# Kernel tuning notes

Measured on AMD Instinct MI355X. Metric: run time of the kernel, lower is better.

The kernel has to match this reference:

```python
import math
import jax, jax.numpy as jnp
import numpy as np

EPS = 1e-7
TOPK = 10
FACTOR_IOU = 6.0
FACTOR_CLS = 0.5


def ciou(b1, b2):
    """Complete IoU. b1, b2 broadcastable [..., 4] boxes (x1,y1,x2,y2)."""
    xi1 = jnp.maximum(b1[..., 0], b2[..., 0])
    yi1 = jnp.maximum(b1[..., 1], b2[..., 1])
    xi2 = jnp.minimum(b1[..., 2], b2[..., 2])
    yi2 = jnp.minimum(b1[..., 3], b2[..., 3])
    inter = jnp.clip(xi2 - xi1, 0) * jnp.clip(yi2 - yi1, 0)
    a1 = (b1[..., 2] - b1[..., 0]) * (b1[..., 3] - b1[..., 1])
    a2 = (b2[..., 2] - b2[..., 0]) * (b2[..., 3] - b2[..., 1])
    union = a1 + a2 - inter
    iou = inter / (union + EPS)
    cx1 = (b1[..., 2] + b1[..., 0]) * 0.5
    cy1 = (b1[..., 3] + b1[..., 1]) * 0.5
    cx2 = (b2[..., 2] + b2[..., 0]) * 0.5
    cy2 = (b2[..., 3] + b2[..., 1]) * 0.5
    cent = (cx1 - cx2) ** 2 + (cy1 - cy2) ** 2
    cw = jnp.maximum(b1[..., 2], b2[..., 2]) - jnp.minimum(b1[..., 0], b2[..., 0])
    ch = jnp.maximum(b1[..., 3], b2[..., 3]) - jnp.minimum(b1[..., 1], b2[..., 1])
    diag = cw ** 2 + ch ** 2 + EPS
    diou = iou - cent / diag
    arctan = (jnp.arctan((b1[..., 2] - b1[..., 0]) / (b1[..., 3] - b1[..., 1] + EPS))
              - jnp.arctan((b2[..., 2] - b2[..., 0]) / (b2[..., 3] - b2[..., 1] + EPS)))
    v = (4.0 / math.pi ** 2) * arctan ** 2
    alpha = jax.lax.stop_gradient(v / (v - iou + 1.0 + EPS))
    return diou - alpha * v


def box_matcher(target, predict_cls, predict_bbox, anchors, class_num):
    """target [B,T,5]; predict_cls [B,A,C] logits; predict_bbox [B,A,4]; anchors [A,2].
    Returns anchor_matched_targets [B,A,C+4], valid_mask [B,A] bool."""
    B, T = target.shape[0], target.shape[1]
    A = anchors.shape[0]
    tcls = jnp.clip(target[..., 0].astype(jnp.int32), 0)        # [B,T]
    tbox = target[..., 1:5]                                       # [B,T,4]

    # grid mask: anchor center inside target box
    ax = anchors[None, None, :, 0]
    ay = anchors[None, None, :, 1]
    grid_mask = ((tbox[:, :, None, 0] < ax) & (ax < tbox[:, :, None, 2])
                 & (tbox[:, :, None, 1] < ay) & (ay < tbox[:, :, None, 3]))  # [B,T,A]

    # pairwise CIoU target x anchor
    iou_mat = jnp.clip(ciou(tbox[:, :, None, :], predict_bbox[:, None, :, :]), 0.0, 1.0)  # [B,T,A]

    # class prob of each target's class at each anchor
    pc = jax.nn.sigmoid(predict_cls)                              # [B,A,C]
    idx_bta = jnp.broadcast_to(tcls[:, :, None], (B, T, A))
    cls_mat = jnp.take_along_axis(pc.transpose(0, 2, 1), idx_bta, axis=1)  # [B,T,A]

    target_matrix = grid_mask * iou_mat ** FACTOR_IOU * cls_mat ** FACTOR_CLS

    # top-k targets per anchor (topk over anchor axis, as in source)
    vals, idx = jax.lax.top_k(target_matrix, TOPK)                # [B,T,K]
    bi = jnp.arange(B)[:, None, None]
    ti = jnp.arange(T)[None, :, None]
    topk_targets = jnp.zeros_like(target_matrix).at[bi, ti, idx].set(vals)
    topk_mask = (topk_targets > 0).astype(jnp.int32)              # [B,T,A]

    # resolve anchors assigned to multiple targets by max IoU
    duplicates = (topk_mask.sum(1, keepdims=True) > 1)            # [B,1,A]
    max_idx = jax.nn.one_hot(jnp.argmax(iou_mat, axis=1), T, dtype=jnp.int32).transpose(0, 2, 1)  # [B,T,A]
    topk_mask = jnp.where(duplicates, max_idx, topk_mask)
    unique_indices = jnp.argmax(topk_mask, axis=1)                # [B,A]
    valid = topk_mask.sum(1)                                      # [B,A]

    align_bbox = jnp.take_along_axis(tbox, jnp.broadcast_to(unique_indices[:, :, None], (B, A, 4)), axis=1)  # [B,A,4]
    align_cls_idx = jnp.take_along_axis(tcls, unique_indices, axis=1)  # [B,A]
    align_cls = jax.nn.one_hot(align_cls_idx, class_num, dtype=target_matrix.dtype)  # [B,A,C]

    iou_m = iou_mat * topk_mask
    tm_m = target_matrix * topk_mask
    max_target = tm_m.max(axis=-1, keepdims=True)                 # [B,T,1]
    max_iou = iou_m.max(axis=-1, keepdims=True)                   # [B,T,1]
    normalize_term = tm_m / (max_target + 1e-9) * max_iou         # [B,T,A]
    normalize_term = jnp.take_along_axis(normalize_term.transpose(0, 2, 1),
                                         unique_indices[:, :, None], axis=2)  # [B,A,1]
    align_cls = align_cls * normalize_term * valid[:, :, None].astype(align_cls.dtype)
    anchor_matched_targets = jnp.concatenate([align_cls, align_bbox], axis=-1)
    return anchor_matched_targets, (valid > 0)


def setup_inputs() -> dict:
    key = jax.random.key(0)
    ks = jax.random.split(key, 6)
    B, T, C = 32, 64, 80
    img = 640.0
    cells = []
    for s in (8, 16, 32):
        n = 640 // s
        xs = (np.arange(n, dtype=np.float32) + 0.5) * s
        gx, gy = np.meshgrid(xs, xs)
        cells.append(np.stack([gx.ravel(), gy.ravel()], axis=1))
    anchors = jnp.asarray(np.concatenate(cells, 0), dtype=jnp.float32)  # [8400,2]
    A = anchors.shape[0]
    cls = jax.random.randint(ks[0], (B, T, 1), 0, C).astype(jnp.float32)
    cxy = jax.random.uniform(ks[1], (B, T, 2)) * img
    wh = jax.random.uniform(ks[2], (B, T, 2)) * 160.0 + 8.0
    tbox = jnp.concatenate([cxy - wh / 2, cxy + wh / 2], axis=-1)
    target = jnp.concatenate([cls, tbox], axis=-1)                # [B,T,5]
    predict_cls = jax.random.normal(ks[3], (B, A, C), dtype=jnp.float32)
    pcxy = anchors[None] + (jax.random.uniform(ks[4], (B, A, 2)) - 0.5) * 32.0
    pwh = jax.random.uniform(ks[5], (B, A, 2)) * 128.0 + 8.0
    predict_bbox = jnp.concatenate([pcxy - pwh / 2, pcxy + pwh / 2], axis=-1)  # [B,A,4]
    return {"target": target, "predict_cls": predict_cls,
            "predict_bbox": predict_bbox, "anchors": anchors}


def reference(target, predict_cls, predict_bbox, anchors):
    C = predict_cls.shape[-1]
    # matcher runs on detached predictions (as in the torch source)
    amt, valid = box_matcher(target,
                             jax.lax.stop_gradient(predict_cls),
                             jax.lax.stop_gradient(predict_bbox),
                             anchors, C)
    targets_cls = amt[..., :C]                                    # [B,A,C]
    targets_bbox = amt[..., C:]                                   # [B,A,4]
    cls_norm = jnp.maximum(targets_cls.sum(), 1.0)
    box_norm = targets_cls.sum(-1)                                # [B,A]

    # BCE-with-logits, sum / cls_norm
    x, t = predict_cls, targets_cls
    bce = jnp.maximum(x, 0) - x * t + jnp.log1p(jnp.exp(-jnp.abs(x)))
    loss_cls = bce.sum() / cls_norm

    # CIoU box loss over valid anchors (elementwise == diag of picked pairwise)
    iou_e = ciou(predict_bbox, targets_bbox)                      # [B,A]
    loss_iou = ((1.0 - iou_e) * box_norm * valid).sum() / cls_norm

    return jnp.stack([loss_iou, loss_cls])
```

## Files before the change

### kernel.cpp

```cpp
#include <hip/hip_runtime.h>
#include <climits>
#include <cmath>


#define NB 32
#define NT 64
#define NA 8400
#define NC 80
#define KTOP 10
#define NE (NT * KTOP)
#define CAP 1024
#define EPSF 1e-7f
#define INV_PI2 0.40528473456935108577f
#define LOG2E_F 1.44269504088896340736f
#define LN2_F   0.69314718055994530942f

__device__ __forceinline__ float atan_wh(float x1, float y1, float x2, float y2) {
  return atanf((x2 - x1) / (y2 - y1 + EPSF));
}

__device__ __forceinline__ float ciou_pair(
    float ax1, float ay1, float ax2, float ay2, float atA,
    float bx1, float by1, float bx2, float by2, float atB)
{
  float xi1 = fmaxf(ax1, bx1), yi1 = fmaxf(ay1, by1);
  float xi2 = fminf(ax2, bx2), yi2 = fminf(ay2, by2);
  float inter = fmaxf(xi2 - xi1, 0.f) * fmaxf(yi2 - yi1, 0.f);
  float a1 = (ax2 - ax1) * (ay2 - ay1);
  float a2 = (bx2 - bx1) * (by2 - by1);
  float iou = inter / (a1 + a2 - inter + EPSF);
  float dcx = (ax2 + ax1) * 0.5f - (bx2 + bx1) * 0.5f;
  float dcy = (ay2 + ay1) * 0.5f - (by2 + by1) * 0.5f;
  float cent = dcx * dcx + dcy * dcy;
  float cw = fmaxf(ax2, bx2) - fminf(ax1, bx1);
  float ch = fmaxf(ay2, by2) - fminf(ay1, by1);
  float diag = cw * cw + ch * ch + EPSF;
  float dv = atA - atB;
  float v = INV_PI2 * dv * dv;
  float alpha = v / (v - iou + 1.f + EPSF);
  return iou - cent / diag - alpha * v;
}

__device__ __forceinline__ float softplus_fast(float x) {
  float e = exp2f(-LOG2E_F * fabsf(x));
  float l = __log2f(1.f + e);
  return fmaxf(x, 0.f) + LN2_F * l;
}

__global__ __launch_bounds__(256) void k_topk(
    const float* __restrict__ target,
    const float* __restrict__ pcls,
    const float* __restrict__ pbox,
    float* __restrict__ top_val, int* __restrict__ top_idx,
    float* __restrict__ top_iou,
    unsigned* __restrict__ mtg, unsigned* __restrict__ mig)
{
  int row = blockIdx.x;
  int tid = threadIdx.x;
  if (tid == 0) { mtg[row] = 0u; mig[row] = 0u; }
  int b = row >> 6;
  const float* tg = target + (size_t)row * 5;
  float tcf = tg[0];
  float x1 = tg[1], y1 = tg[2], x2 = tg[3], y2 = tg[4];
  int tc = (int)tcf; tc = tc < 0 ? 0 : (tc > NC - 1 ? NC - 1 : tc);
  float atan_t = atan_wh(x1, y1, x2, y2);

  __shared__ int s_n;
  __shared__ float s_val[CAP];
  __shared__ int s_idx[CAP];
  __shared__ float xw_v[4];  __shared__ int xw_a[4];
  __shared__ float w_val[KTOP]; __shared__ int w_idx[KTOP];
  if (tid == 0) s_n = 0;
  __syncthreads();

  const float* pb_b = pbox + (size_t)b * NA * 4;
  const float* pc_b = pcls + (size_t)b * NA * NC;

#define LEVEL_LOOP(S, N, BASE)                                              \
  {                                                                         \
    const float s = (float)(S);                                             \
    \
    int ix0 = (int)floorf(x1 / s - 0.5f); ix0 = ix0 < 0 ? 0 : ix0;          \
    int ix1 = (int)ceilf (x2 / s - 0.5f); ix1 = ix1 > (N)-1 ? (N)-1 : ix1;  \
    int iy0 = (int)floorf(y1 / s - 0.5f); iy0 = iy0 < 0 ? 0 : iy0;          \
    int iy1 = (int)ceilf (y2 / s - 0.5f); iy1 = iy1 > (N)-1 ? (N)-1 : iy1;  \
    int w = ix1 - ix0 + 1; w = w < 0 ? 0 : w;                               \
    int h = iy1 - iy0 + 1; h = h < 0 ? 0 : h;                               \
    int cnt = w * h;                                                        \
    for (int k = tid; k < cnt; k += 256) {                                  \
      int ix = ix0 + k % w;                                                 \
      int iy = iy0 + k / w;                                                 \
      float anx = (ix + 0.5f) * s;                                          \
      float any_ = (iy + 0.5f) * s;                                         \
      if (x1 < anx && anx < x2 && y1 < any_ && any_ < y2) {                 \
        int a = (BASE) + iy * (N) + ix;                                     \
        float4 bb = ((const float4*)pb_b)[a];                               \
        float c = ciou_pair(x1, y1, x2, y2, atan_t, bb.x, bb.y, bb.z, bb.w, \
                            atan_wh(bb.x, bb.y, bb.z, bb.w));               \
        float io = fminf(fmaxf(c, 0.f), 1.f);                               \
        float i2 = io * io;                                                 \
        float i6 = i2 * i2 * i2;                                            \
        float sc = pc_b[(size_t)a * NC + tc];                               \
        float sig = 1.f / (1.f + expf(-sc));                                \
        float tm = i6 * sqrtf(sig);                                         \
        int slot = atomicAdd(&s_n, 1);                                      \
        if (slot < CAP) { s_val[slot] = tm; s_idx[slot] = a; }              \
      }                                                                     \
    }                                                                       \
  }
  LEVEL_LOOP(8, 80, 0)
  LEVEL_LOOP(16, 40, 6400)
  LEVEL_LOOP(32, 20, 8000)
#undef LEVEL_LOOP
  __syncthreads();
  int n = s_n; if (n > CAP) n = CAP;

  float v0 = -1.f, v1 = -1.f, v2 = -1.f, v3 = -1.f;
  int a0 = INT_MAX, a1 = INT_MAX, a2 = INT_MAX, a3 = INT_MAX;
  if (tid < n)       { v0 = s_val[tid];       a0 = s_idx[tid]; }
  if (tid + 256 < n) { v1 = s_val[tid + 256]; a1 = s_idx[tid + 256]; }
  if (tid + 512 < n) { v2 = s_val[tid + 512]; a2 = s_idx[tid + 512]; }
  if (tid + 768 < n) { v3 = s_val[tid + 768]; a3 = s_idx[tid + 768]; }

  for (int k = 0; k < KTOP; k++) {
    float bv = v0; int ba = a0;
    if (v1 > bv || (v1 == bv && a1 < ba)) { bv = v1; ba = a1; }
    if (v2 > bv || (v2 == bv && a2 < ba)) { bv = v2; ba = a2; }
    if (v3 > bv || (v3 == bv && a3 < ba)) { bv = v3; ba = a3; }
#pragma unroll
    for (int off = 32; off > 0; off >>= 1) {
      float ov = __shfl_xor(bv, off); int oa = __shfl_xor(ba, off);
      if (ov > bv || (ov == bv && oa < ba)) { bv = ov; ba = oa; }
    }
    if ((tid & 63) == 0) { xw_v[tid >> 6] = bv; xw_a[tid >> 6] = ba; }
    __syncthreads();
    float fv = xw_v[0]; int fa = xw_a[0];
    { float ov = xw_v[1]; int oa = xw_a[1];
      if (ov > fv || (ov == fv && oa < fa)) { fv = ov; fa = oa; } }
    { float ov = xw_v[2]; int oa = xw_a[2];
      if (ov > fv || (ov == fv && oa < fa)) { fv = ov; fa = oa; } }
    { float ov = xw_v[3]; int oa = xw_a[3];
      if (ov > fv || (ov == fv && oa < fa)) { fv = ov; fa = oa; } }
    if (tid == 0) { w_val[k] = fv; w_idx[k] = fa; }
    if (a0 == fa) { v0 = -1.f; a0 = INT_MAX; }
    if (a1 == fa) { v1 = -1.f; a1 = INT_MAX; }
    if (a2 == fa) { v2 = -1.f; a2 = INT_MAX; }
    if (a3 == fa) { v3 = -1.f; a3 = INT_MAX; }
    __syncthreads();
  }

  if (tid < KTOP) {
    int k = tid;
    int ai = w_idx[k]; float v = w_val[k];
    float io = 0.f;
    if (ai != INT_MAX && v > 0.f) {
      float4 bb = ((const float4*)pb_b)[ai];
      float c = ciou_pair(x1, y1, x2, y2, atan_t, bb.x, bb.y, bb.z, bb.w,
                          atan_wh(bb.x, bb.y, bb.z, bb.w));
      io = fminf(fmaxf(c, 0.f), 1.f);
    } else { ai = -1; v = 0.f; }
    size_t o = (size_t)row * KTOP + k;
    top_val[o] = v; top_idx[o] = ai; top_iou[o] = io;
  }
}

__global__ __launch_bounds__(256) void k_resolve(
    const float* __restrict__ target, const float* __restrict__ pcls,
    const float* __restrict__ pbox, const float* __restrict__ anchors,
    const float* __restrict__ top_val, const int* __restrict__ top_idx,
    const float* __restrict__ top_iou,
    float* __restrict__ as_tm, float* __restrict__ as_x,
    float* __restrict__ as_cio, int* __restrict__ as_u,
    unsigned* __restrict__ mtg, unsigned* __restrict__ mig)
{
  int gid = blockIdx.x * 256 + threadIdx.x;
  int entry = gid >> 6;
  int lane = threadIdx.x & 63;
  int b = entry / NE;
  int el = entry - b * NE;

  const float* bv = top_val + (size_t)b * NE;
  const int* bix = top_idx + (size_t)b * NE;
  float v = bv[el];
  int a = bix[el];

  bool dead = (v <= 0.f);
  int cnt = 0, first = NE;
  if (!dead) {
    for (int s = lane; s < NE; s += 64) {
      float v2 = bv[s]; int a2 = bix[s];
      if (v2 > 0.f && a2 == a) { cnt++; if (s < first) first = s; }
    }
    for (int off = 32; off > 0; off >>= 1) {
      cnt += __shfl_xor(cnt, off);
      int of = __shfl_xor(first, off);
      first = of < first ? of : first;
    }
    if (first != el) dead = true;
  }
  if (dead) {
    if (lane == 0) { as_tm[entry] = 0.f; as_x[entry] = 0.f;
                     as_cio[entry] = 0.f; as_u[entry] = 0; }
    return;
  }

  const float* pb = pbox + ((size_t)b * NA + a) * 4;
  int u; float tm = -1.f, io;
  if (cnt == 1) {
    u = el / KTOP; tm = v; io = top_iou[entry];
  } else {
    const float* tg = target + (size_t)(b * NT + lane) * 5;
    float tx1 = tg[1], ty1 = tg[2], tx2 = tg[3], ty2 = tg[4];
    float ta = atan_wh(tx1, ty1, tx2, ty2);
    float bx1 = pb[0], by1 = pb[1], bx2 = pb[2], by2 = pb[3];
    float pa = atan_wh(bx1, by1, bx2, by2);
    float c = ciou_pair(tx1, ty1, tx2, ty2, ta, bx1, by1, bx2, by2, pa);
    float cc = fminf(fmaxf(c, 0.f), 1.f);
    float best = cc; int bu = lane;
    for (int off = 32; off > 0; off >>= 1) {
      float ob = __shfl_xor(best, off);
      int ou = __shfl_xor(bu, off);
      if (ob > best || (ob == best && ou < bu)) { best = ob; bu = ou; }
    }
    u = bu; io = best;
  }

  if (lane == 0) {
    const float* tgu = target + (size_t)(b * NT + u) * 5;
    float ux1 = tgu[1], uy1 = tgu[2], ux2 = tgu[3], uy2 = tgu[4];
    int cu = (int)tgu[0]; cu = cu < 0 ? 0 : (cu > NC - 1 ? NC - 1 : cu);
    float x = pcls[((size_t)b * NA + a) * NC + cu];
    if (cnt != 1) {
      float2 an = ((const float2*)anchors)[a];
      float gm = (ux1 < an.x && an.x < ux2 && uy1 < an.y && an.y < uy2) ? 1.f : 0.f;
      float i2 = io * io; float i6 = i2 * i2 * i2;
      float sig = 1.f / (1.f + expf(-x));
      tm = gm * i6 * sqrtf(sig);
    }
    float bx1 = pb[0], by1 = pb[1], bx2 = pb[2], by2 = pb[3];
    float c = ciou_pair(ux1, uy1, ux2, uy2, atan_wh(ux1, uy1, ux2, uy2),
                        bx1, by1, bx2, by2, atan_wh(bx1, by1, bx2, by2));
    as_tm[entry] = tm; as_x[entry] = x; as_cio[entry] = 1.f - c; as_u[entry] = u;
    atomicMax(&mtg[b * NT + u], __float_as_uint(tm));
    atomicMax(&mig[b * NT + u], __float_as_uint(io));
  }
}

#define BCE_BLOCKS 2048
__global__ __launch_bounds__(256) void k_bce_sums(
    const float* __restrict__ pcls,
    const float* __restrict__ as_tm, const float* __restrict__ as_x,
    const float* __restrict__ as_cio, const int* __restrict__ as_u,
    const unsigned* __restrict__ mtg, const unsigned* __restrict__ mig,
    double* __restrict__ bce_part, double* __restrict__ k2_part)
{
  int tid = threadIdx.x;
  __shared__ double red[256];

  if (blockIdx.x < BCE_BLOCKS) {
    const float4* p4 = (const float4*)pcls;
    const int n4 = NB * NA * NC / 4;
    double acc = 0.0;
    for (int i = blockIdx.x * 256 + tid; i < n4; i += BCE_BLOCKS * 256) {
      float4 v = p4[i];
      float p = (softplus_fast(v.x) + softplus_fast(v.y)) +
                (softplus_fast(v.z) + softplus_fast(v.w));
      acc += (double)p;
    }
    red[tid] = acc; __syncthreads();
    for (int off = 128; off > 0; off >>= 1) {
      if (tid < off) red[tid] += red[tid + off];
      __syncthreads();
    }
    if (tid == 0) bce_part[blockIdx.x] = red[0];
    return;
  }

  int b = blockIdx.x - BCE_BLOCKS;
  double s1 = 0.0, s2 = 0.0, s3 = 0.0;
  for (int e = tid; e < NE; e += 256) {
    size_t o = (size_t)b * NE + e;
    float tm = as_tm[o];
    int u = as_u[o];
    float maxt = __uint_as_float(mtg[b * NT + u]);
    float maxi = __uint_as_float(mig[b * NT + u]);
    float nrm = tm / (maxt + 1e-9f) * maxi;
    s1 += (double)nrm;
    s2 += (double)as_x[o] * (double)nrm;
    s3 += (double)(as_cio[o] * nrm);
  }
  red[tid] = s1; __syncthreads();
  for (int off = 128; off > 0; off >>= 1) {
    if (tid < off) red[tid] += red[tid + off];
    __syncthreads();
  }
  if (tid == 0) k2_part[b * 3 + 0] = red[0];
  __syncthreads();
  red[tid] = s2; __syncthreads();
  for (int off = 128; off > 0; off >>= 1) {
    if (tid < off) red[tid] += red[tid + off];
    __syncthreads();
  }
  if (tid == 0) k2_part[b * 3 + 1] = red[0];
  __syncthreads();
  red[tid] = s3; __syncthreads();
  for (int off = 128; off > 0; off >>= 1) {
    if (tid < off) red[tid] += red[tid + off];
    __syncthreads();
  }
  if (tid == 0) k2_part[b * 3 + 2] = red[0];
}

__global__ __launch_bounds__(256) void k_final(const double* __restrict__ bce_part,
                                               const double* __restrict__ k2_part,
                                               float* __restrict__ out) {
  __shared__ double red[256];
  int tid = threadIdx.x;
  double s = 0.0;
  for (int i = tid; i < BCE_BLOCKS; i += 256) s += bce_part[i];
  red[tid] = s; __syncthreads();
  for (int off = 128; off > 0; off >>= 1) {
    if (tid < off) red[tid] += red[tid + off];
    __syncthreads();
  }
  double s4 = red[0]; __syncthreads();

  red[tid] = (tid < NB) ? k2_part[3 * tid + 0] : 0.0; __syncthreads();
  for (int off = 128; off > 0; off >>= 1) {
    if (tid < off) red[tid] += red[tid + off];
    __syncthreads();
  }
  double s1 = red[0]; __syncthreads();

  red[tid] = (tid < NB) ? k2_part[3 * tid + 1] : 0.0; __syncthreads();
  for (int off = 128; off > 0; off >>= 1) {
    if (tid < off) red[tid] += red[tid + off];
    __syncthreads();
  }
  double s2 = red[0]; __syncthreads();

  red[tid] = (tid < NB) ? k2_part[3 * tid + 2] : 0.0; __syncthreads();
  for (int off = 128; off > 0; off >>= 1) {
    if (tid < off) red[tid] += red[tid + off];
    __syncthreads();
  }
  double s3 = red[0];

  if (tid == 0) {
    double cn = fmax(s1, 1.0);
    out[0] = (float)(s3 / cn);
    out[1] = (float)((s4 - s2) / cn);
  }
}

extern "C" void kernel_launch(void* const* d_in, const int* in_sizes, int n_in,
                              void* d_out, int out_size, void* d_ws, size_t ws_size,
                              hipStream_t stream) {
  const float* target  = (const float*)d_in[0];
  const float* pcls    = (const float*)d_in[1];
  const float* pbox    = (const float*)d_in[2];
  const float* anchors = (const float*)d_in[3];
  float* out = (float*)d_out;

  char* ws = (char*)d_ws;
  float*    top_val = (float*)ws;
  int*      top_idx = (int*)(ws + 81920);
  float*    top_iou = (float*)(ws + 163840);
  float*    as_tm   = (float*)(ws + 245760);
  float*    as_x    = (float*)(ws + 327680);
  float*    as_cio  = (float*)(ws + 409600);
  int*      as_u    = (int*)(ws + 491520);
  unsigned* mtg     = (unsigned*)(ws + 573440);
  unsigned* mig     = (unsigned*)(ws + 581632);
  double*   k2_part = (double*)(ws + 589824);
  double*   k3_part = (double*)(ws + 590592);

  k_topk<<<NB * NT, 256, 0, stream>>>(target, pcls, pbox,
                                      top_val, top_idx, top_iou, mtg, mig);
  k_resolve<<<(NB * NE * 64) / 256, 256, 0, stream>>>(
      target, pcls, pbox, anchors, top_val, top_idx, top_iou,
      as_tm, as_x, as_cio, as_u, mtg, mig);
  k_bce_sums<<<BCE_BLOCKS + NB, 256, 0, stream>>>(
      pcls, as_tm, as_x, as_cio, as_u, mtg, mig, k3_part, k2_part);
  k_final<<<1, 256, 0, stream>>>(k3_part, k2_part, out);
}
```

Baseline: 80.06 us.

## Fuse BCE pass into top-k kernel and fold final reduce via ticket

Moves the dense softplus/BCE reduction over all class logits into the first kernel, so it runs alongside the per-target top-k blocks instead of after resolve. The per-batch sums kernel now ends with an atomic ticket counter, and the last block performs the global final reduction, which removes the separate single-block final launch. This drops one launch and gives the bandwidth-heavy BCE pass latency-bound top-k work to overlap with. The cost is a larger first grid in which the BCE blocks are scheduled first and may delay the top-k blocks, plus a dependence on a threadfence/atomic last-block pattern.

```diff
diff --git a/kernel.cpp b/kernel.cpp
--- a/kernel.cpp
+++ b/kernel.cpp
@@ -14,6 +14,7 @@
 #define INV_PI2 0.40528473456935108577f
 #define LOG2E_F 1.44269504088896340736f
 #define LN2_F   0.69314718055994530942f
+#define BCE_BLOCKS 2048
 
 __device__ __forceinline__ float atan_wh(float x1, float y1, float x2, float y2) {
   return atanf((x2 - x1) / (y2 - y1 + EPSF));
@@ -47,16 +48,39 @@
   return fmaxf(x, 0.f) + LN2_F * l;
 }
 
-__global__ __launch_bounds__(256) void k_topk(
+__global__ __launch_bounds__(256) void k_bce_topk(
     const float* __restrict__ target,
     const float* __restrict__ pcls,
     const float* __restrict__ pbox,
     float* __restrict__ top_val, int* __restrict__ top_idx,
     float* __restrict__ top_iou,
-    unsigned* __restrict__ mtg, unsigned* __restrict__ mig)
+    unsigned* __restrict__ mtg, unsigned* __restrict__ mig,
+    double* __restrict__ bce_part, unsigned* __restrict__ ticket)
 {
-  int row = blockIdx.x;
   int tid = threadIdx.x;
+  __shared__ double red[256];
+
+  if (blockIdx.x < BCE_BLOCKS) {
+    if (blockIdx.x == 0 && tid == 0) *ticket = 0u;
+    const float4* p4 = (const float4*)pcls;
+    const int n4 = NB * NA * NC / 4;
+    double acc = 0.0;
+    for (int i = blockIdx.x * 256 + tid; i < n4; i += BCE_BLOCKS * 256) {
+      float4 v = p4[i];
+      float p = (softplus_fast(v.x) + softplus_fast(v.y)) +
+                (softplus_fast(v.z) + softplus_fast(v.w));
+      acc += (double)p;
+    }
+    red[tid] = acc; __syncthreads();
+    for (int off = 128; off > 0; off >>= 1) {
+      if (tid < off) red[tid] += red[tid + off];
+      __syncthreads();
+    }
+    if (tid == 0) bce_part[blockIdx.x] = red[0];
+    return;
+  }
+
+  int row = blockIdx.x - BCE_BLOCKS;
   if (tid == 0) { mtg[row] = 0u; mig[row] = 0u; }
   int b = row >> 6;
   const float* tg = target + (size_t)row * 5;
@@ -79,7 +103,6 @@
 #define LEVEL_LOOP(S, N, BASE)                                              \
   {                                                                         \
     const float s = (float)(S);                                             \
-    \
     int ix0 = (int)floorf(x1 / s - 0.5f); ix0 = ix0 < 0 ? 0 : ix0;          \
     int ix1 = (int)ceilf (x2 / s - 0.5f); ix1 = ix1 > (N)-1 ? (N)-1 : ix1;  \
     int iy0 = (int)floorf(y1 / s - 0.5f); iy0 = iy0 < 0 ? 0 : iy0;          \
@@ -246,37 +269,19 @@
   }
 }
 
-#define BCE_BLOCKS 2048
-__global__ __launch_bounds__(256) void k_bce_sums(
-    const float* __restrict__ pcls,
+__global__ __launch_bounds__(256) void k_sums_final(
     const float* __restrict__ as_tm, const float* __restrict__ as_x,
     const float* __restrict__ as_cio, const int* __restrict__ as_u,
     const unsigned* __restrict__ mtg, const unsigned* __restrict__ mig,
-    double* __restrict__ bce_part, double* __restrict__ k2_part)
+    const double* __restrict__ bce_part,
+    double* __restrict__ k2_part, unsigned* __restrict__ ticket,
+    float* __restrict__ out)
 {
+  int b = blockIdx.x;
   int tid = threadIdx.x;
   __shared__ double red[256];
-
-  if (blockIdx.x < BCE_BLOCKS) {
-    const float4* p4 = (const float4*)pcls;
-    const int n4 = NB * NA * NC / 4;
-    double acc = 0.0;
-    for (int i = blockIdx.x * 256 + tid; i < n4; i += BCE_BLOCKS * 256) {
-      float4 v = p4[i];
-      float p = (softplus_fast(v.x) + softplus_fast(v.y)) +
-                (softplus_fast(v.z) + softplus_fast(v.w));
-      acc += (double)p;
-    }
-    red[tid] = acc; __syncthreads();
-    for (int off = 128; off > 0; off >>= 1) {
-      if (tid < off) red[tid] += red[tid + off];
-      __syncthreads();
-    }
-    if (tid == 0) bce_part[blockIdx.x] = red[0];
-    return;
-  }
-
-  int b = blockIdx.x - BCE_BLOCKS;
+  __shared__ int lastflag;
+
   double s1 = 0.0, s2 = 0.0, s3 = 0.0;
   for (int e = tid; e < NE; e += 256) {
     size_t o = (size_t)b * NE + e;
@@ -309,13 +314,17 @@
     __syncthreads();
   }
   if (tid == 0) k2_part[b * 3 + 2] = red[0];
-}
-
-__global__ __launch_bounds__(256) void k_final(const double* __restrict__ bce_part,
-                                               const double* __restrict__ k2_part,
-                                               float* __restrict__ out) {
-  __shared__ double red[256];
-  int tid = threadIdx.x;
+  __syncthreads();
+
+  if (tid == 0) {
+    __threadfence();
+    unsigned old = atomicAdd(ticket, 1u);
+    lastflag = (old == NB - 1) ? 1 : 0;
+  }
+  __syncthreads();
+  if (!lastflag) return;
+  __threadfence();
+
   double s = 0.0;
   for (int i = tid; i < BCE_BLOCKS; i += 256) s += bce_part[i];
   red[tid] = s; __syncthreads();
@@ -330,26 +339,26 @@
     if (tid < off) red[tid] += red[tid + off];
     __syncthreads();
   }
-  double s1 = red[0]; __syncthreads();
+  double t1 = red[0]; __syncthreads();
 
   red[tid] = (tid < NB) ? k2_part[3 * tid + 1] : 0.0; __syncthreads();
   for (int off = 128; off > 0; off >>= 1) {
     if (tid < off) red[tid] += red[tid + off];
     __syncthreads();
   }
-  double s2 = red[0]; __syncthreads();
+  double t2 = red[0]; __syncthreads();
 
   red[tid] = (tid < NB) ? k2_part[3 * tid + 2] : 0.0; __syncthreads();
   for (int off = 128; off > 0; off >>= 1) {
     if (tid < off) red[tid] += red[tid + off];
     __syncthreads();
   }
-  double s3 = red[0];
+  double t3 = red[0];
 
   if (tid == 0) {
-    double cn = fmax(s1, 1.0);
-    out[0] = (float)(s3 / cn);
-    out[1] = (float)((s4 - s2) / cn);
+    double cn = fmax(t1, 1.0);
+    out[0] = (float)(t3 / cn);
+    out[1] = (float)((s4 - t2) / cn);
   }
 }
 
@@ -374,13 +383,14 @@
   unsigned* mig     = (unsigned*)(ws + 581632);
   double*   k2_part = (double*)(ws + 589824);
   double*   k3_part = (double*)(ws + 590592);
-
-  k_topk<<<NB * NT, 256, 0, stream>>>(target, pcls, pbox,
-                                      top_val, top_idx, top_iou, mtg, mig);
+  unsigned* ticket  = (unsigned*)(ws + 606976);
+
+  k_bce_topk<<<BCE_BLOCKS + NB * NT, 256, 0, stream>>>(
+      target, pcls, pbox, top_val, top_idx, top_iou, mtg, mig,
+      k3_part, ticket);
   k_resolve<<<(NB * NE * 64) / 256, 256, 0, stream>>>(
       target, pcls, pbox, anchors, top_val, top_idx, top_iou,
       as_tm, as_x, as_cio, as_u, mtg, mig);
-  k_bce_sums<<<BCE_BLOCKS + NB, 256, 0, stream>>>(
-      pcls, as_tm, as_x, as_cio, as_u, mtg, mig, k3_part, k2_part);
-  k_final<<<1, 256, 0, stream>>>(k3_part, k2_part, out);
-}
+  k_sums_final<<<NB, 256, 0, stream>>>(
+      as_tm, as_x, as_cio, as_u, mtg, mig, k3_part, k2_part, ticket, out);
+}
```

Result: no change. 80.82 us (+1.0%).

## Prune class-score loads with IoU-only top-k threshold before exact top-k

Applied to the files above, without the earlier changes.

The candidate pass now stores only the IoU^6 term and skips the per-anchor class-logit gather and sigmoid. A first top-k over IoU^6 gives a lower bound on the tenth-best alignment score. Only candidates whose IoU^6 reaches that bound load the logit and compute the full score, followed by a second top-k. This cuts scattered global loads of pcls, but adds an extra top-k pass with twenty more block barriers and more shared memory.

```diff
diff --git a/kernel.cpp b/kernel.cpp
--- a/kernel.cpp
+++ b/kernel.cpp
@@ -14,6 +14,7 @@
 #define INV_PI2 0.40528473456935108577f
 #define LOG2E_F 1.44269504088896340736f
 #define LN2_F   0.69314718055994530942f
+#define BCE_BLOCKS 2048
 
 __device__ __forceinline__ float atan_wh(float x1, float y1, float x2, float y2) {
   return atanf((x2 - x1) / (y2 - y1 + EPSF));
@@ -66,10 +67,12 @@
   float atan_t = atan_wh(x1, y1, x2, y2);
 
   __shared__ int s_n;
-  __shared__ float s_val[CAP];
+  __shared__ float s_i6[CAP];
+  __shared__ float s_tm[CAP];
   __shared__ int s_idx[CAP];
   __shared__ float xw_v[4];  __shared__ int xw_a[4];
   __shared__ float w_val[KTOP]; __shared__ int w_idx[KTOP];
+  __shared__ float s_thr;
   if (tid == 0) s_n = 0;
   __syncthreads();
 
@@ -79,11 +82,10 @@
 #define LEVEL_LOOP(S, N, BASE)                                              \
   {                                                                         \
     const float s = (float)(S);                                             \
-    \
-    int ix0 = (int)floorf(x1 / s - 0.5f); ix0 = ix0 < 0 ? 0 : ix0;          \
-    int ix1 = (int)ceilf (x2 / s - 0.5f); ix1 = ix1 > (N)-1 ? (N)-1 : ix1;  \
-    int iy0 = (int)floorf(y1 / s - 0.5f); iy0 = iy0 < 0 ? 0 : iy0;          \
-    int iy1 = (int)ceilf (y2 / s - 0.5f); iy1 = iy1 > (N)-1 ? (N)-1 : iy1;  \
+    int ix0 = (int)floorf(x1 / s - 0.5f); if (ix0 < 0) ix0 = 0;             \
+    int ix1 = (int)ceilf (x2 / s - 0.5f); if (ix1 > (N)-1) ix1 = (N)-1;     \
+    int iy0 = (int)floorf(y1 / s - 0.5f); if (iy0 < 0) iy0 = 0;             \
+    int iy1 = (int)ceilf (y2 / s - 0.5f); if (iy1 > (N)-1) iy1 = (N)-1;     \
     int w = ix1 - ix0 + 1; w = w < 0 ? 0 : w;                               \
     int h = iy1 - iy0 + 1; h = h < 0 ? 0 : h;                               \
     int cnt = w * h;                                                        \
@@ -100,11 +102,8 @@
         float io = fminf(fmaxf(c, 0.f), 1.f);                               \
         float i2 = io * io;                                                 \
         float i6 = i2 * i2 * i2;                                            \
-        float sc = pc_b[(size_t)a * NC + tc];                               \
-        float sig = 1.f / (1.f + expf(-sc));                                \
-        float tm = i6 * sqrtf(sig);                                         \
         int slot = atomicAdd(&s_n, 1);                                      \
-        if (slot < CAP) { s_val[slot] = tm; s_idx[slot] = a; }              \
+        if (slot < CAP) { s_i6[slot] = i6; s_idx[slot] = a; }               \
       }                                                                     \
     }                                                                       \
   }
@@ -115,38 +114,106 @@
   __syncthreads();
   int n = s_n; if (n > CAP) n = CAP;
 
-  float v0 = -1.f, v1 = -1.f, v2 = -1.f, v3 = -1.f;
-  int a0 = INT_MAX, a1 = INT_MAX, a2 = INT_MAX, a3 = INT_MAX;
-  if (tid < n)       { v0 = s_val[tid];       a0 = s_idx[tid]; }
-  if (tid + 256 < n) { v1 = s_val[tid + 256]; a1 = s_idx[tid + 256]; }
-  if (tid + 512 < n) { v2 = s_val[tid + 512]; a2 = s_idx[tid + 512]; }
-  if (tid + 768 < n) { v3 = s_val[tid + 768]; a3 = s_idx[tid + 768]; }
-
-  for (int k = 0; k < KTOP; k++) {
-    float bv = v0; int ba = a0;
-    if (v1 > bv || (v1 == bv && a1 < ba)) { bv = v1; ba = a1; }
-    if (v2 > bv || (v2 == bv && a2 < ba)) { bv = v2; ba = a2; }
-    if (v3 > bv || (v3 == bv && a3 < ba)) { bv = v3; ba = a3; }
+  {
+    float v0 = -1.f, v1 = -1.f, v2 = -1.f, v3 = -1.f;
+    int a0 = INT_MAX, a1 = INT_MAX, a2 = INT_MAX, a3 = INT_MAX;
+    if (tid < n)       { v0 = s_i6[tid];       a0 = s_idx[tid]; }
+    if (tid + 256 < n) { v1 = s_i6[tid + 256]; a1 = s_idx[tid + 256]; }
+    if (tid + 512 < n) { v2 = s_i6[tid + 512]; a2 = s_idx[tid + 512]; }
+    if (tid + 768 < n) { v3 = s_i6[tid + 768]; a3 = s_idx[tid + 768]; }
+    for (int k = 0; k < KTOP; k++) {
+      float bv = v0; int ba = a0;
+      if (v1 > bv || (v1 == bv && a1 < ba)) { bv = v1; ba = a1; }
+      if (v2 > bv || (v2 == bv && a2 < ba)) { bv = v2; ba = a2; }
+      if (v3 > bv || (v3 == bv && a3 < ba)) { bv = v3; ba = a3; }
 #pragma unroll
-    for (int off = 32; off > 0; off >>= 1) {
-      float ov = __shfl_xor(bv, off); int oa = __shfl_xor(ba, off);
-      if (ov > bv || (ov == bv && oa < ba)) { bv = ov; ba = oa; }
-    }
-    if ((tid & 63) == 0) { xw_v[tid >> 6] = bv; xw_a[tid >> 6] = ba; }
-    __syncthreads();
-    float fv = xw_v[0]; int fa = xw_a[0];
-    { float ov = xw_v[1]; int oa = xw_a[1];
-      if (ov > fv || (ov == fv && oa < fa)) { fv = ov; fa = oa; } }
-    { float ov = xw_v[2]; int oa = xw_a[2];
-      if (ov > fv || (ov == fv && oa < fa)) { fv = ov; fa = oa; } }
-    { float ov = xw_v[3]; int oa = xw_a[3];
-      if (ov > fv || (ov == fv && oa < fa)) { fv = ov; fa = oa; } }
-    if (tid == 0) { w_val[k] = fv; w_idx[k] = fa; }
-    if (a0 == fa) { v0 = -1.f; a0 = INT_MAX; }
-    if (a1 == fa) { v1 = -1.f; a1 = INT_MAX; }
-    if (a2 == fa) { v2 = -1.f; a2 = INT_MAX; }
-    if (a3 == fa) { v3 = -1.f; a3 = INT_MAX; }
-    __syncthreads();
+      for (int off = 32; off > 0; off >>= 1) {
+        float ov = __shfl_xor(bv, off); int oa = __shfl_xor(ba, off);
+        if (ov > bv || (ov == bv && oa < ba)) { bv = ov; ba = oa; }
+      }
+      if ((tid & 63) == 0) { xw_v[tid >> 6] = bv; xw_a[tid >> 6] = ba; }
+      __syncthreads();
+      float fv = xw_v[0]; int fa = xw_a[0];
+      { float ov = xw_v[1]; int oa = xw_a[1];
+        if (ov > fv || (ov == fv && oa < fa)) { fv = ov; fa = oa; } }
+      { float ov = xw_v[2]; int oa = xw_a[2];
+        if (ov > fv || (ov == fv && oa < fa)) { fv = ov; fa = oa; } }
+      { float ov = xw_v[3]; int oa = xw_a[3];
+        if (ov > fv || (ov == fv && oa < fa)) { fv = ov; fa = oa; } }
+      if (tid == 0) { w_val[k] = fv; w_idx[k] = fa; }
+      if (a0 == fa) { v0 = -1.f; a0 = INT_MAX; }
+      if (a1 == fa) { v1 = -1.f; a1 = INT_MAX; }
+      if (a2 == fa) { v2 = -1.f; a2 = INT_MAX; }
+      if (a3 == fa) { v3 = -1.f; a3 = INT_MAX; }
+      __syncthreads();
+    }
+  }
+
+  if (tid == 0) {
+    float thr;
+    if (n < KTOP) {
+      thr = -1.f;
+    } else {
+      thr = 3.402823466e+38f;
+      for (int k = 0; k < KTOP; k++) {
+        int a = w_idx[k];
+        float sc = pc_b[(size_t)a * NC + tc];
+        float sig = 1.f / (1.f + expf(-sc));
+        float tm = w_val[k] * sqrtf(sig);
+        thr = fminf(thr, tm);
+      }
+    }
+    s_thr = thr;
+  }
+  __syncthreads();
+  float thr = s_thr;
+
+  for (int e = tid; e < n; e += 256) {
+    float i6 = s_i6[e];
+    if (i6 >= thr) {
+      int a = s_idx[e];
+      float sc = pc_b[(size_t)a * NC + tc];
+      float sig = 1.f / (1.f + expf(-sc));
+      s_tm[e] = i6 * sqrtf(sig);
+    } else {
+      s_tm[e] = -1.f;
+    }
+  }
+  __syncthreads();
+
+  {
+    float v0 = -1.f, v1 = -1.f, v2 = -1.f, v3 = -1.f;
+    int a0 = INT_MAX, a1 = INT_MAX, a2 = INT_MAX, a3 = INT_MAX;
+    if (tid < n)       { v0 = s_tm[tid];       a0 = s_idx[tid]; }
+    if (tid + 256 < n) { v1 = s_tm[tid + 256]; a1 = s_idx[tid + 256]; }
+    if (tid + 512 < n) { v2 = s_tm[tid + 512]; a2 = s_idx[tid + 512]; }
+    if (tid + 768 < n) { v3 = s_tm[tid + 768]; a3 = s_idx[tid + 768]; }
+    for (int k = 0; k < KTOP; k++) {
+      float bv = v0; int ba = a0;
+      if (v1 > bv || (v1 == bv && a1 < ba)) { bv = v1; ba = a1; }
+      if (v2 > bv || (v2 == bv && a2 < ba)) { bv = v2; ba = a2; }
+      if (v3 > bv || (v3 == bv && a3 < ba)) { bv = v3; ba = a3; }
+#pragma unroll
+      for (int off = 32; off > 0; off >>= 1) {
+        float ov = __shfl_xor(bv, off); int oa = __shfl_xor(ba, off);
+        if (ov > bv || (ov == bv && oa < ba)) { bv = ov; ba = oa; }
+      }
+      if ((tid & 63) == 0) { xw_v[tid >> 6] = bv; xw_a[tid >> 6] = ba; }
+      __syncthreads();
+      float fv = xw_v[0]; int fa = xw_a[0];
+      { float ov = xw_v[1]; int oa = xw_a[1];
+        if (ov > fv || (ov == fv && oa < fa)) { fv = ov; fa = oa; } }
+      { float ov = xw_v[2]; int oa = xw_a[2];
+        if (ov > fv || (ov == fv && oa < fa)) { fv = ov; fa = oa; } }
+      { float ov = xw_v[3]; int oa = xw_a[3];
+        if (ov > fv || (ov == fv && oa < fa)) { fv = ov; fa = oa; } }
+      if (tid == 0) { w_val[k] = fv; w_idx[k] = fa; }
+      if (a0 == fa) { v0 = -1.f; a0 = INT_MAX; }
+      if (a1 == fa) { v1 = -1.f; a1 = INT_MAX; }
+      if (a2 == fa) { v2 = -1.f; a2 = INT_MAX; }
+      if (a3 == fa) { v3 = -1.f; a3 = INT_MAX; }
+      __syncthreads();
+    }
   }
 
   if (tid < KTOP) {
@@ -246,7 +313,6 @@
   }
 }
 
-#define BCE_BLOCKS 2048
 __global__ __launch_bounds__(256) void k_bce_sums(
     const float* __restrict__ pcls,
     const float* __restrict__ as_tm, const float* __restrict__ as_x,
```

Measured after the change: 97.87 us. 1.22x slower.

## Pack top-k keys into u64, batch 4 entries per wave in resolve

Applied to the files above, without the earlier changes.

The top-k selection in k_topk now packs score and inverted anchor index into a single 64-bit key, so each reduction step is one u64 max instead of paired float/int compares and shuffles. k_resolve handles four entries per wavefront and shares one scan over the batch's top-k list, cutting its launched waves by four. Sigmoid uses an exp2-based fast form. The packing relies on non-negative scores ordering correctly as uint bits, and the per-wave batching serializes more work per wave.

```diff
diff --git a/kernel.cpp b/kernel.cpp
--- a/kernel.cpp
+++ b/kernel.cpp
@@ -14,6 +14,9 @@
 #define INV_PI2 0.40528473456935108577f
 #define LOG2E_F 1.44269504088896340736f
 #define LN2_F   0.69314718055994530942f
+#define BCE_BLOCKS 2048
+
+typedef unsigned long long u64;
 
 __device__ __forceinline__ float atan_wh(float x1, float y1, float x2, float y2) {
   return atanf((x2 - x1) / (y2 - y1 + EPSF));
@@ -47,6 +50,14 @@
   return fmaxf(x, 0.f) + LN2_F * l;
 }
 
+__device__ __forceinline__ float sigmoid_fast(float x) {
+  return 1.f / (1.f + exp2f(-LOG2E_F * x));
+}
+
+__device__ __forceinline__ u64 pack_key(float tm, int a) {
+  return ((u64)__float_as_uint(tm) << 32) | (unsigned)(INT_MAX - a);
+}
+
 __global__ __launch_bounds__(256) void k_topk(
     const float* __restrict__ target,
     const float* __restrict__ pcls,
@@ -66,10 +77,9 @@
   float atan_t = atan_wh(x1, y1, x2, y2);
 
   __shared__ int s_n;
-  __shared__ float s_val[CAP];
-  __shared__ int s_idx[CAP];
-  __shared__ float xw_v[4];  __shared__ int xw_a[4];
-  __shared__ float w_val[KTOP]; __shared__ int w_idx[KTOP];
+  __shared__ u64 s_key[CAP];
+  __shared__ u64 xw_k[4];
+  __shared__ u64 w_key[KTOP];
   if (tid == 0) s_n = 0;
   __syncthreads();
 
@@ -79,11 +89,10 @@
 #define LEVEL_LOOP(S, N, BASE)                                              \
   {                                                                         \
     const float s = (float)(S);                                             \
-    \
-    int ix0 = (int)floorf(x1 / s - 0.5f); ix0 = ix0 < 0 ? 0 : ix0;          \
-    int ix1 = (int)ceilf (x2 / s - 0.5f); ix1 = ix1 > (N)-1 ? (N)-1 : ix1;  \
-    int iy0 = (int)floorf(y1 / s - 0.5f); iy0 = iy0 < 0 ? 0 : iy0;          \
-    int iy1 = (int)ceilf (y2 / s - 0.5f); iy1 = iy1 > (N)-1 ? (N)-1 : iy1;  \
+    int ix0 = (int)floorf(x1 / s - 0.5f); if (ix0 < 0) ix0 = 0;             \
+    int ix1 = (int)ceilf (x2 / s - 0.5f); if (ix1 > (N)-1) ix1 = (N)-1;     \
+    int iy0 = (int)floorf(y1 / s - 0.5f); if (iy0 < 0) iy0 = 0;             \
+    int iy1 = (int)ceilf (y2 / s - 0.5f); if (iy1 > (N)-1) iy1 = (N)-1;     \
     int w = ix1 - ix0 + 1; w = w < 0 ? 0 : w;                               \
     int h = iy1 - iy0 + 1; h = h < 0 ? 0 : h;                               \
     int cnt = w * h;                                                        \
@@ -101,10 +110,9 @@
         float i2 = io * io;                                                 \
         float i6 = i2 * i2 * i2;                                            \
         float sc = pc_b[(size_t)a * NC + tc];                               \
-        float sig = 1.f / (1.f + expf(-sc));                                \
-        float tm = i6 * sqrtf(sig);                                         \
+        float tm = i6 * sqrtf(sigmoid_fast(sc));                            \
         int slot = atomicAdd(&s_n, 1);                                      \
-        if (slot < CAP) { s_val[slot] = tm; s_idx[slot] = a; }              \
+        if (slot < CAP) s_key[slot] = pack_key(tm, a);                      \
       }                                                                     \
     }                                                                       \
   }
@@ -115,45 +123,45 @@
   __syncthreads();
   int n = s_n; if (n > CAP) n = CAP;
 
-  float v0 = -1.f, v1 = -1.f, v2 = -1.f, v3 = -1.f;
-  int a0 = INT_MAX, a1 = INT_MAX, a2 = INT_MAX, a3 = INT_MAX;
-  if (tid < n)       { v0 = s_val[tid];       a0 = s_idx[tid]; }
-  if (tid + 256 < n) { v1 = s_val[tid + 256]; a1 = s_idx[tid + 256]; }
-  if (tid + 512 < n) { v2 = s_val[tid + 512]; a2 = s_idx[tid + 512]; }
-  if (tid + 768 < n) { v3 = s_val[tid + 768]; a3 = s_idx[tid + 768]; }
+  u64 k0 = 0, k1 = 0, k2 = 0, k3 = 0;
+  if (tid < n)       k0 = s_key[tid];
+  if (tid + 256 < n) k1 = s_key[tid + 256];
+  if (tid + 512 < n) k2 = s_key[tid + 512];
+  if (tid + 768 < n) k3 = s_key[tid + 768];
 
   for (int k = 0; k < KTOP; k++) {
-    float bv = v0; int ba = a0;
-    if (v1 > bv || (v1 == bv && a1 < ba)) { bv = v1; ba = a1; }
-    if (v2 > bv || (v2 == bv && a2 < ba)) { bv = v2; ba = a2; }
-    if (v3 > bv || (v3 == bv && a3 < ba)) { bv = v3; ba = a3; }
+    u64 bk = k0;
+    if (k1 > bk) bk = k1;
+    if (k2 > bk) bk = k2;
+    if (k3 > bk) bk = k3;
 #pragma unroll
     for (int off = 32; off > 0; off >>= 1) {
-      float ov = __shfl_xor(bv, off); int oa = __shfl_xor(ba, off);
-      if (ov > bv || (ov == bv && oa < ba)) { bv = ov; ba = oa; }
-    }
-    if ((tid & 63) == 0) { xw_v[tid >> 6] = bv; xw_a[tid >> 6] = ba; }
-    __syncthreads();
-    float fv = xw_v[0]; int fa = xw_a[0];
-    { float ov = xw_v[1]; int oa = xw_a[1];
-      if (ov > fv || (ov == fv && oa < fa)) { fv = ov; fa = oa; } }
-    { float ov = xw_v[2]; int oa = xw_a[2];
-      if (ov > fv || (ov == fv && oa < fa)) { fv = ov; fa = oa; } }
-    { float ov = xw_v[3]; int oa = xw_a[3];
-      if (ov > fv || (ov == fv && oa < fa)) { fv = ov; fa = oa; } }
-    if (tid == 0) { w_val[k] = fv; w_idx[k] = fa; }
-    if (a0 == fa) { v0 = -1.f; a0 = INT_MAX; }
-    if (a1 == fa) { v1 = -1.f; a1 = INT_MAX; }
-    if (a2 == fa) { v2 = -1.f; a2 = INT_MAX; }
-    if (a3 == fa) { v3 = -1.f; a3 = INT_MAX; }
+      u64 ok = __shfl_xor(bk, off);
+      if (ok > bk) bk = ok;
+    }
+    if ((tid & 63) == 0) xw_k[tid >> 6] = bk;
+    __syncthreads();
+    u64 fk = xw_k[0];
+    if (xw_k[1] > fk) fk = xw_k[1];
+    if (xw_k[2] > fk) fk = xw_k[2];
+    if (xw_k[3] > fk) fk = xw_k[3];
+    if (tid == 0) w_key[k] = fk;
+    if (fk != 0) {
+      if (k0 == fk) k0 = 0;
+      if (k1 == fk) k1 = 0;
+      if (k2 == fk) k2 = 0;
+      if (k3 == fk) k3 = 0;
+    }
     __syncthreads();
   }
 
   if (tid < KTOP) {
     int k = tid;
-    int ai = w_idx[k]; float v = w_val[k];
+    u64 key = w_key[k];
+    float v = __uint_as_float((unsigned)(key >> 32));
+    int ai = INT_MAX - (int)(key & 0xFFFFFFFFu);
     float io = 0.f;
-    if (ai != INT_MAX && v > 0.f) {
+    if (key != 0 && v > 0.f) {
       float4 bb = ((const float4*)pb_b)[ai];
       float c = ciou_pair(x1, y1, x2, y2, atan_t, bb.x, bb.y, bb.z, bb.w,
                           atan_wh(bb.x, bb.y, bb.z, bb.w));
@@ -173,80 +181,97 @@
     float* __restrict__ as_cio, int* __restrict__ as_u,
     unsigned* __restrict__ mtg, unsigned* __restrict__ mig)
 {
-  int gid = blockIdx.x * 256 + threadIdx.x;
-  int entry = gid >> 6;
+  int wave = (blockIdx.x * 256 + threadIdx.x) >> 6;
   int lane = threadIdx.x & 63;
-  int b = entry / NE;
-  int el = entry - b * NE;
+  int e0 = wave * 4;
+  int b = e0 / NE;
 
   const float* bv = top_val + (size_t)b * NE;
   const int* bix = top_idx + (size_t)b * NE;
-  float v = bv[el];
-  int a = bix[el];
-
-  bool dead = (v <= 0.f);
-  int cnt = 0, first = NE;
-  if (!dead) {
-    for (int s = lane; s < NE; s += 64) {
-      float v2 = bv[s]; int a2 = bix[s];
-      if (v2 > 0.f && a2 == a) { cnt++; if (s < first) first = s; }
-    }
+
+  int ea[4]; float ev[4];
+  bool dead[4];
+  int cnt[4]; int first[4];
+#pragma unroll
+  for (int j = 0; j < 4; j++) {
+    int el = (e0 - b * NE) + j;
+    ev[j] = bv[el]; ea[j] = bix[el];
+    dead[j] = (ev[j] <= 0.f);
+    cnt[j] = 0; first[j] = NE;
+  }
+
+  for (int s = lane; s < NE; s += 64) {
+    float v2 = bv[s]; int a2 = bix[s];
+    bool live = (v2 > 0.f);
+#pragma unroll
+    for (int j = 0; j < 4; j++) {
+      if (live && a2 == ea[j]) { cnt[j]++; if (s < first[j]) first[j] = s; }
+    }
+  }
+#pragma unroll
+  for (int j = 0; j < 4; j++) {
     for (int off = 32; off > 0; off >>= 1) {
-      cnt += __shfl_xor(cnt, off);
-      int of = __shfl_xor(first, off);
-      first = of < first ? of : first;
-    }
-    if (first != el) dead = true;
-  }
-  if (dead) {
-    if (lane == 0) { as_tm[entry] = 0.f; as_x[entry] = 0.f;
-                     as_cio[entry] = 0.f; as_u[entry] = 0; }
-    return;
-  }
-
-  const float* pb = pbox + ((size_t)b * NA + a) * 4;
-  int u; float tm = -1.f, io;
-  if (cnt == 1) {
-    u = el / KTOP; tm = v; io = top_iou[entry];
-  } else {
-    const float* tg = target + (size_t)(b * NT + lane) * 5;
-    float tx1 = tg[1], ty1 = tg[2], tx2 = tg[3], ty2 = tg[4];
-    float ta = atan_wh(tx1, ty1, tx2, ty2);
-    float bx1 = pb[0], by1 = pb[1], bx2 = pb[2], by2 = pb[3];
-    float pa = atan_wh(bx1, by1, bx2, by2);
-    float c = ciou_pair(tx1, ty1, tx2, ty2, ta, bx1, by1, bx2, by2, pa);
-    float cc = fminf(fmaxf(c, 0.f), 1.f);
-    float best = cc; int bu = lane;
-    for (int off = 32; off > 0; off >>= 1) {
-      float ob = __shfl_xor(best, off);
-      int ou = __shfl_xor(bu, off);
-      if (ob > best || (ob == best && ou < bu)) { best = ob; bu = ou; }
-    }
-    u = bu; io = best;
-  }
-
-  if (lane == 0) {
-    const float* tgu = target + (size_t)(b * NT + u) * 5;
-    float ux1 = tgu[1], uy1 = tgu[2], ux2 = tgu[3], uy2 = tgu[4];
-    int cu = (int)tgu[0]; cu = cu < 0 ? 0 : (cu > NC - 1 ? NC - 1 : cu);
-    float x = pcls[((size_t)b * NA + a) * NC + cu];
-    if (cnt != 1) {
-      float2 an = ((const float2*)anchors)[a];
-      float gm = (ux1 < an.x && an.x < ux2 && uy1 < an.y && an.y < uy2) ? 1.f : 0.f;
-      float i2 = io * io; float i6 = i2 * i2 * i2;
-      float sig = 1.f / (1.f + expf(-x));
-      tm = gm * i6 * sqrtf(sig);
-    }
-    float bx1 = pb[0], by1 = pb[1], bx2 = pb[2], by2 = pb[3];
-    float c = ciou_pair(ux1, uy1, ux2, uy2, atan_wh(ux1, uy1, ux2, uy2),
-                        bx1, by1, bx2, by2, atan_wh(bx1, by1, bx2, by2));
-    as_tm[entry] = tm; as_x[entry] = x; as_cio[entry] = 1.f - c; as_u[entry] = u;
-    atomicMax(&mtg[b * NT + u], __float_as_uint(tm));
-    atomicMax(&mig[b * NT + u], __float_as_uint(io));
-  }
-}
-
-#define BCE_BLOCKS 2048
+      cnt[j] += __shfl_xor(cnt[j], off);
+      int of = __shfl_xor(first[j], off);
+      first[j] = of < first[j] ? of : first[j];
+    }
+  }
+
+#pragma unroll
+  for (int j = 0; j < 4; j++) {
+    int entry = e0 + j;
+    int el = (e0 - b * NE) + j;
+    if (!dead[j] && first[j] != el) dead[j] = true;
+    if (dead[j]) {
+      if (lane == 0) { as_tm[entry] = 0.f; as_x[entry] = 0.f;
+                       as_cio[entry] = 0.f; as_u[entry] = 0; }
+      continue;
+    }
+    int a = ea[j];
+    const float* pb = pbox + ((size_t)b * NA + a) * 4;
+    int u; float tm = -1.f, io;
+    if (cnt[j] == 1) {
+      u = el / KTOP; tm = ev[j]; io = top_iou[entry];
+    } else {
+      const float* tg = target + (size_t)(b * NT + lane) * 5;
+      float tx1 = tg[1], ty1 = tg[2], tx2 = tg[3], ty2 = tg[4];
+      float ta = atan_wh(tx1, ty1, tx2, ty2);
+      float bx1 = pb[0], by1 = pb[1], bx2 = pb[2], by2 = pb[3];
+      float pa = atan_wh(bx1, by1, bx2, by2);
+      float c = ciou_pair(tx1, ty1, tx2, ty2, ta, bx1, by1, bx2, by2, pa);
+      float cc = fminf(fmaxf(c, 0.f), 1.f);
+      float best = cc; int bu = lane;
+      for (int off = 32; off > 0; off >>= 1) {
+        float ob = __shfl_xor(best, off);
+        int ou = __shfl_xor(bu, off);
+        if (ob > best || (ob == best && ou < bu)) { best = ob; bu = ou; }
+      }
+      u = bu; io = best;
+    }
+
+    if (lane == 0) {
+      const float* tgu = target + (size_t)(b * NT + u) * 5;
+      float ux1 = tgu[1], uy1 = tgu[2], ux2 = tgu[3], uy2 = tgu[4];
+      int cu = (int)tgu[0]; cu = cu < 0 ? 0 : (cu > NC - 1 ? NC - 1 : cu);
+      float x = pcls[((size_t)b * NA + a) * NC + cu];
+      if (cnt[j] != 1) {
+        float2 an = ((const float2*)anchors)[a];
+        float gm = (ux1 < an.x && an.x < ux2 && uy1 < an.y && an.y < uy2)
+                       ? 1.f : 0.f;
+        float i2 = io * io; float i6 = i2 * i2 * i2;
+        float sig = sigmoid_fast(x);
+        tm = gm * i6 * sqrtf(sig);
+      }
+      float bx1 = pb[0], by1 = pb[1], bx2 = pb[2], by2 = pb[3];
+      float c = ciou_pair(ux1, uy1, ux2, uy2, atan_wh(ux1, uy1, ux2, uy2),
+                          bx1, by1, bx2, by2, atan_wh(bx1, by1, bx2, by2));
+      as_tm[entry] = tm; as_x[entry] = x; as_cio[entry] = 1.f - c; as_u[entry] = u;
+      atomicMax(&mtg[b * NT + u], __float_as_uint(tm));
+      atomicMax(&mig[b * NT + u], __float_as_uint(io));
+    }
+  }
+}
+
 __global__ __launch_bounds__(256) void k_bce_sums(
     const float* __restrict__ pcls,
     const float* __restrict__ as_tm, const float* __restrict__ as_x,
@@ -377,7 +402,7 @@
 
   k_topk<<<NB * NT, 256, 0, stream>>>(target, pcls, pbox,
                                       top_val, top_idx, top_iou, mtg, mig);
-  k_resolve<<<(NB * NE * 64) / 256, 256, 0, stream>>>(
+  k_resolve<<<(NB * NE / 4 * 64) / 256, 256, 0, stream>>>(
       target, pcls, pbox, anchors, top_val, top_idx, top_iou,
       as_tm, as_x, as_cio, as_u, mtg, mig);
   k_bce_sums<<<BCE_BLOCKS + NB, 256, 0, stream>>>(
```

After: 78.02 us. 1.03x faster.
